# Optimization experiments

Measured on AMD Instinct MI355X. Metric: run time of the kernel, lower is better.

The kernel has to match this reference:

```python
import jax, jax.numpy as jnp
import numpy as np

B, T, N, D, H, S, L, O = 32, 12, 2048, 2, 64, 2, 2, 1


def setup_inputs() -> dict:
    key = jax.random.key(0)
    ks = jax.random.split(key, 32)
    inp = {}
    inp["x"] = jax.random.normal(ks[0], (B, T, N, D), dtype=jnp.float32)
    sup = jax.random.uniform(ks[1], (S, N, N), dtype=jnp.float32)
    # row-normalized, like random-walk diffusion transition matrices
    inp["supports"] = sup / jnp.sum(sup, axis=-1, keepdims=True)
    i = 2
    for l in range(L):
        din = (D if l == 0 else H) + H  # concat([x, h]) width
        for g in ("r", "u", "c"):
            inp[f"W{g}{l}"] = jax.random.normal(ks[i], (din, H), dtype=jnp.float32) * 0.02; i += 1
            inp[f"b{g}{l}"] = jnp.zeros((H,), jnp.float32)
        inp[f"Wd{l}"] = jax.random.normal(ks[i], (S, H, H), dtype=jnp.float32) * 0.02; i += 1
        inp[f"bd{l}"] = jnp.zeros((S, H), jnp.float32)
    inp["Wo"] = jax.random.normal(ks[i], (H, O), dtype=jnp.float32) * 0.02
    inp["bo"] = jnp.zeros((O,), jnp.float32)
    return inp


def _cell(x_t, h, supports, Wr, br, Wu, bu, Wc, bc, Wd, bd):
    # x_t: [B,N,din-H], h: [B,N,H]
    xh = jnp.concatenate([x_t, h], axis=-1)
    r = jax.nn.sigmoid(xh @ Wr + br)  # computed but unused, as in the source module
    u = jax.nn.sigmoid(xh @ Wu + bu)
    c = jnp.tanh(xh @ Wc + bc)
    # Diffusion conv is DEAD CODE in the source (h_diff never used); kept for fidelity,
    # DCE'd under jit. snm,bmh,shk -> per-support graph matmul + linear, summed.
    h_diff = h + jnp.einsum('snm,bmh,shk->bnk', supports, h, Wd) + jnp.sum(bd, axis=0)
    del r, h_diff
    return u * h + (1.0 - u) * c


def reference(x, supports,
              Wr0, br0, Wu0, bu0, Wc0, bc0, Wd0, bd0,
              Wr1, br1, Wu1, bu1, Wc1, bc1, Wd1, bd1,
              Wo, bo):
    p0 = (Wr0, br0, Wu0, bu0, Wc0, bc0, Wd0, bd0)
    p1 = (Wr1, br1, Wu1, bu1, Wc1, bc1, Wd1, bd1)

    def step(carry, x_t):
        h0, h1 = carry
        h0 = _cell(x_t, h0, supports, *p0)
        h1 = _cell(h0, h1, supports, *p1)  # dropout p=0.0 -> identity
        return (h0, h1), None

    h_init = (jnp.zeros((B, N, H), x.dtype), jnp.zeros((B, N, H), x.dtype))
    (h0, h1), _ = jax.lax.scan(step, h_init, jnp.swapaxes(x, 0, 1))  # scan over T
    return h1 @ Wo + bo  # [B, N, O]
```

## Files before the change

kernel.cpp:

```cpp
#include <hip/hip_runtime.h>


#define TSTEPS 12

__device__ __forceinline__ float fsig(float z) {
    z = fminf(fmaxf(z, -30.f), 30.f);
    return 1.f / (1.f + __expf(-z));
}
__device__ __forceinline__ float ftanh(float z) {
    z = fminf(fmaxf(z, -15.f), 15.f);
    float e = __expf(2.f * z);
    return 1.f - 2.f / (e + 1.f);
}


__global__ void pack_weights(const float* __restrict__ Wu0, const float* __restrict__ bu0,
                             const float* __restrict__ Wc0, const float* __restrict__ bc0,
                             const float* __restrict__ Wu1, const float* __restrict__ bu1,
                             const float* __restrict__ Wc1, const float* __restrict__ bc1,
                             const float* __restrict__ Wo, const float* __restrict__ bo,
                             float* __restrict__ Wp) {
    const int tid = blockIdx.x * blockDim.x + threadIdx.x;
    const int nthr = gridDim.x * blockDim.x;
    for (int i = tid; i < 256; i += nthr) {
        const int k = i >> 7, r = i & 127, wv = r >> 5, j = r & 31;
        const int col = wv * 16 + (j & 15);
        Wp[i] = (j < 16) ? Wu0[k * 64 + col] : Wc0[k * 64 + col];
    }
    for (int i = tid; i < 8192; i += nthr) {
        const int k = i >> 7, r = i & 127, wv = r >> 5, j = r & 31;
        const int col = wv * 16 + (j & 15);
        Wp[256 + i] = (j < 16) ? Wu0[(2 + k) * 64 + col] : Wc0[(2 + k) * 64 + col];
    }
    for (int i = tid; i < 16384; i += nthr) {
        const int k = i >> 7, r = i & 127, wv = r >> 5, j = r & 31;
        const int col = wv * 16 + (j & 15);
        Wp[8448 + i] = (j < 16) ? Wu1[k * 64 + col] : Wc1[k * 64 + col];
    }
    for (int i = tid; i < 128; i += nthr) {
        const int wv = i >> 5, j = i & 31;
        const int col = wv * 16 + (j & 15);
        Wp[24832 + i] = (j < 16) ? bu0[col] : bc0[col];
        Wp[24960 + i] = (j < 16) ? bu1[col] : bc1[col];
    }
    for (int i = tid; i < 64; i += nthr) Wp[25088 + i] = Wo[i];
    if (tid == 0) Wp[25152] = bo[0];
}

#define REP16(X) X(0) X(1) X(2) X(3) X(4) X(5) X(6) X(7) \
                 X(8) X(9) X(10) X(11) X(12) X(13) X(14) X(15)

#define INITJ(J) zu##J = bp_[J]; zc##J = bp_[16 + J];
#define FMAJ(J)  zu##J = __builtin_fmaf(hk_, wk_[J], zu##J); \
                 zc##J = __builtin_fmaf(hk_, wk_[16 + J], zc##J);
#define XPJ(J)   zu##J = __builtin_fmaf(xv.x, wx_[J], zu##J); \
                 zu##J = __builtin_fmaf(xv.y, wx_[128 + J], zu##J); \
                 zc##J = __builtin_fmaf(xv.x, wx_[16 + J], zc##J); \
                 zc##J = __builtin_fmaf(xv.y, wx_[128 + 16 + J], zc##J);
#define ACTJ(J)  { const float u_ = fsig(zu##J); const float c_ = ftanh(zc##J); \
                   zu##J = __builtin_fmaf(u_, hb_[(J) * 64], (1.f - u_) * c_); }
#define STJ(J)   hb_[(J) * 64] = zu##J;
#define KSTEP(AR, WB, KK) { const float hk_ = (AR)[(KK) * 64]; \
                            const float* wk_ = (WB) + (size_t)(KK) * 128; REP16(FMAJ) }
#define POJ(J)   part = __builtin_fmaf(zu##J, wo_[J], part);

__global__ __launch_bounds__(256, 4) void dcrnn_main(const float* __restrict__ x,
                                                     const float* __restrict__ Wp,
                                                     float* __restrict__ out) {
    __shared__ float A[128 * 64];
    __shared__ float P[4 * 64];

    const int tid = threadIdx.x;
    const int lane = tid & 63;
    const int w = __builtin_amdgcn_readfirstlane(tid >> 6);

    const int s0 = blockIdx.x * 64;
    const int b = s0 >> 11;
    const int n0 = s0 & 2047;

    const float* Wxw = Wp + w * 32;
    const float* W0w = Wp + 256 + w * 32;
    const float* W1w = Wp + 8448 + w * 32;
    const float* B0w = Wp + 24832 + w * 32;
    const float* B1w = Wp + 24960 + w * 32;

    for (int i = tid; i < 128 * 64; i += 256) A[i] = 0.f;
    __syncthreads();

    const float* Arow = A + lane;
    const float* xlane = x + (size_t)(b * TSTEPS) * 4096 + (size_t)(n0 + lane) * 2;
    float* hb0 = &A[(w * 16) * 64 + lane];
    float* hb1 = &A[(64 + w * 16) * 64 + lane];

    float zu0, zu1, zu2, zu3, zu4, zu5, zu6, zu7;
    float zu8, zu9, zu10, zu11, zu12, zu13, zu14, zu15;
    float zc0, zc1, zc2, zc3, zc4, zc5, zc6, zc7;
    float zc8, zc9, zc10, zc11, zc12, zc13, zc14, zc15;

#pragma unroll 1
    for (int t = 0; t < TSTEPS; ++t) {
        const float2 xv = *(const float2*)(xlane + t * 4096);

        { const float* bp_ = B0w; REP16(INITJ) }
#pragma unroll 1
        for (int k = 0; k < 64; k += 4) {
            KSTEP(Arow, W0w, k + 0)
            KSTEP(Arow, W0w, k + 1)
            KSTEP(Arow, W0w, k + 2)
            KSTEP(Arow, W0w, k + 3)
        }
        { const float* wx_ = Wxw; REP16(XPJ) }
        { const float* hb_ = hb0; REP16(ACTJ) }
        __syncthreads();
        { float* hb_ = hb0; REP16(STJ) }
        __syncthreads();

        { const float* bp_ = B1w; REP16(INITJ) }
#pragma unroll 1
        for (int k = 0; k < 128; k += 4) {
            KSTEP(Arow, W1w, k + 0)
            KSTEP(Arow, W1w, k + 1)
            KSTEP(Arow, W1w, k + 2)
            KSTEP(Arow, W1w, k + 3)
        }
        { const float* hb_ = hb1; REP16(ACTJ) }
        __syncthreads();
        { float* hb_ = hb1; REP16(STJ) }
    }

    float part = 0.f;
    { const float* wo_ = Wp + 25088 + w * 16; REP16(POJ) }
    P[w * 64 + lane] = part;
    __syncthreads();
    if (tid < 64) {
        out[s0 + tid] = Wp[25152] + P[tid] + P[64 + tid] + P[128 + tid] + P[192 + tid];
    }
}

extern "C" void kernel_launch(void* const* d_in, const int* in_sizes, int n_in,
                              void* d_out, int out_size, void* d_ws, size_t ws_size,
                              hipStream_t stream) {
    const float* x   = (const float*)d_in[0];
    const float* Wu0 = (const float*)d_in[4];
    const float* bu0 = (const float*)d_in[5];
    const float* Wc0 = (const float*)d_in[6];
    const float* bc0 = (const float*)d_in[7];
    const float* Wu1 = (const float*)d_in[12];
    const float* bu1 = (const float*)d_in[13];
    const float* Wc1 = (const float*)d_in[14];
    const float* bc1 = (const float*)d_in[15];
    const float* Wo  = (const float*)d_in[18];
    const float* bo  = (const float*)d_in[19];

    float* Wp = (float*)d_ws;

    hipLaunchKernelGGL(pack_weights, dim3(64), dim3(256), 0, stream,
                       Wu0, bu0, Wc0, bc0, Wu1, bu1, Wc1, bc1, Wo, bo, Wp);
    hipLaunchKernelGGL(dcrnn_main, dim3(65536 / 64), dim3(256), 0, stream,
                       x, Wp, (float*)d_out);
}
```

Measured before the change: 635.1 us.

## Retile GRU kernel to two nodes per lane and eight output columns per wave

Each block now handles 128 nodes with 512 threads. Each lane owns two adjacent nodes and each wave owns 8 of the 64 hidden columns, where before it was one node and 16 columns. Every weight scalar loaded from global/constant memory is now reused across two nodes, and shared-memory hidden-state reads become float2. This halves per-node weight-load traffic, at the cost of doubling shared memory per block (64KB), which may reduce how many blocks fit on each CU.

```diff
diff --git a/kernel.cpp b/kernel.cpp
--- a/kernel.cpp
+++ b/kernel.cpp
@@ -22,118 +22,146 @@
                              float* __restrict__ Wp) {
     const int tid = blockIdx.x * blockDim.x + threadIdx.x;
     const int nthr = gridDim.x * blockDim.x;
+    for (int i = tid; i < 8192; i += nthr) {
+        const int k = i >> 7, r = i & 127, wv = r >> 4, j = r & 15;
+        const int col = wv * 8 + (j & 7);
+        Wp[i] = (j < 8) ? Wu0[(2 + k) * 64 + col] : Wc0[(2 + k) * 64 + col];
+    }
     for (int i = tid; i < 256; i += nthr) {
-        const int k = i >> 7, r = i & 127, wv = r >> 5, j = r & 31;
-        const int col = wv * 16 + (j & 15);
-        Wp[i] = (j < 16) ? Wu0[k * 64 + col] : Wc0[k * 64 + col];
-    }
-    for (int i = tid; i < 8192; i += nthr) {
-        const int k = i >> 7, r = i & 127, wv = r >> 5, j = r & 31;
-        const int col = wv * 16 + (j & 15);
-        Wp[256 + i] = (j < 16) ? Wu0[(2 + k) * 64 + col] : Wc0[(2 + k) * 64 + col];
+        const int k = i >> 7, r = i & 127, wv = r >> 4, j = r & 15;
+        const int col = wv * 8 + (j & 7);
+        Wp[8192 + i] = (j < 8) ? Wu0[k * 64 + col] : Wc0[k * 64 + col];
     }
     for (int i = tid; i < 16384; i += nthr) {
-        const int k = i >> 7, r = i & 127, wv = r >> 5, j = r & 31;
-        const int col = wv * 16 + (j & 15);
-        Wp[8448 + i] = (j < 16) ? Wu1[k * 64 + col] : Wc1[k * 64 + col];
+        const int k = i >> 7, r = i & 127, wv = r >> 4, j = r & 15;
+        const int col = wv * 8 + (j & 7);
+        Wp[8448 + i] = (j < 8) ? Wu1[k * 64 + col] : Wc1[k * 64 + col];
     }
     for (int i = tid; i < 128; i += nthr) {
-        const int wv = i >> 5, j = i & 31;
-        const int col = wv * 16 + (j & 15);
-        Wp[24832 + i] = (j < 16) ? bu0[col] : bc0[col];
-        Wp[24960 + i] = (j < 16) ? bu1[col] : bc1[col];
+        const int wv = i >> 4, j = i & 15;
+        const int col = wv * 8 + (j & 7);
+        Wp[24832 + i] = (j < 8) ? bu0[col] : bc0[col];
+        Wp[24960 + i] = (j < 8) ? bu1[col] : bc1[col];
     }
     for (int i = tid; i < 64; i += nthr) Wp[25088 + i] = Wo[i];
     if (tid == 0) Wp[25152] = bo[0];
 }
 
-#define REP16(X) X(0) X(1) X(2) X(3) X(4) X(5) X(6) X(7) \
-                 X(8) X(9) X(10) X(11) X(12) X(13) X(14) X(15)
+#define REP8(X) X(0) X(1) X(2) X(3) X(4) X(5) X(6) X(7)
 
-#define INITJ(J) zu##J = bp_[J]; zc##J = bp_[16 + J];
-#define FMAJ(J)  zu##J = __builtin_fmaf(hk_, wk_[J], zu##J); \
-                 zc##J = __builtin_fmaf(hk_, wk_[16 + J], zc##J);
-#define XPJ(J)   zu##J = __builtin_fmaf(xv.x, wx_[J], zu##J); \
-                 zu##J = __builtin_fmaf(xv.y, wx_[128 + J], zu##J); \
-                 zc##J = __builtin_fmaf(xv.x, wx_[16 + J], zc##J); \
-                 zc##J = __builtin_fmaf(xv.y, wx_[128 + 16 + J], zc##J);
-#define ACTJ(J)  { const float u_ = fsig(zu##J); const float c_ = ftanh(zc##J); \
-                   zu##J = __builtin_fmaf(u_, hb_[(J) * 64], (1.f - u_) * c_); }
-#define STJ(J)   hb_[(J) * 64] = zu##J;
-#define KSTEP(AR, WB, KK) { const float hk_ = (AR)[(KK) * 64]; \
-                            const float* wk_ = (WB) + (size_t)(KK) * 128; REP16(FMAJ) }
-#define POJ(J)   part = __builtin_fmaf(zu##J, wo_[J], part);
+#define INITJ(J) zu##J##0 = bp_[J]; zu##J##1 = bp_[J]; \
+                 zc##J##0 = bp_[8 + J]; zc##J##1 = bp_[8 + J];
 
-__global__ __launch_bounds__(256, 4) void dcrnn_main(const float* __restrict__ x,
+#define FMAJ(J) \
+    zu##J##0 = __builtin_fmaf(hv.x, wk_[J], zu##J##0); \
+    zu##J##1 = __builtin_fmaf(hv.y, wk_[J], zu##J##1); \
+    zc##J##0 = __builtin_fmaf(hv.x, wk_[8 + J], zc##J##0); \
+    zc##J##1 = __builtin_fmaf(hv.y, wk_[8 + J], zc##J##1);
+
+#define KSTEP(WB, KK) { \
+    const float2 hv = *(const float2*)(Aptr + (size_t)(KK) * 128); \
+    const float* wk_ = (WB) + (size_t)(KK) * 128; \
+    REP8(FMAJ) }
+
+#define XPJ(J) \
+    zu##J##0 = __builtin_fmaf(xv.x, wx_[J], __builtin_fmaf(xv.y, wx_[128 + J], zu##J##0)); \
+    zu##J##1 = __builtin_fmaf(xv.z, wx_[J], __builtin_fmaf(xv.w, wx_[128 + J], zu##J##1)); \
+    zc##J##0 = __builtin_fmaf(xv.x, wx_[8 + J], __builtin_fmaf(xv.y, wx_[136 + J], zc##J##0)); \
+    zc##J##1 = __builtin_fmaf(xv.z, wx_[8 + J], __builtin_fmaf(xv.w, wx_[136 + J], zc##J##1));
+
+#define ACTJ(J) { \
+    const float2 ho = *(const float2*)(hb_ + (J) * 128); \
+    float u_, c_; \
+    u_ = fsig(zu##J##0); c_ = ftanh(zc##J##0); \
+    zu##J##0 = __builtin_fmaf(u_, ho.x, (1.f - u_) * c_); \
+    u_ = fsig(zu##J##1); c_ = ftanh(zc##J##1); \
+    zu##J##1 = __builtin_fmaf(u_, ho.y, (1.f - u_) * c_); }
+
+#define STJ(J) *(float2*)(hb_ + (J) * 128) = make_float2(zu##J##0, zu##J##1);
+
+#define POJ(J) part0 = __builtin_fmaf(zu##J##0, wo_[J], part0); \
+               part1 = __builtin_fmaf(zu##J##1, wo_[J], part1);
+
+__global__ __launch_bounds__(512, 4) void dcrnn_main(const float* __restrict__ x,
                                                      const float* __restrict__ Wp,
                                                      float* __restrict__ out) {
-    __shared__ float A[128 * 64];
-    __shared__ float P[4 * 64];
+    __shared__ float A[128 * 128];
+    __shared__ float P[8 * 128];
 
     const int tid = threadIdx.x;
     const int lane = tid & 63;
     const int w = __builtin_amdgcn_readfirstlane(tid >> 6);
 
-    const int s0 = blockIdx.x * 64;
+    const int s0 = blockIdx.x * 128;
     const int b = s0 >> 11;
     const int n0 = s0 & 2047;
 
-    const float* Wxw = Wp + w * 32;
-    const float* W0w = Wp + 256 + w * 32;
-    const float* W1w = Wp + 8448 + w * 32;
-    const float* B0w = Wp + 24832 + w * 32;
-    const float* B1w = Wp + 24960 + w * 32;
+    const float* W0w = Wp + w * 16;
+    const float* Wxw = Wp + 8192 + w * 16;
+    const float* W1w = Wp + 8448 + w * 16;
+    const float* B0w = Wp + 24832 + w * 16;
+    const float* B1w = Wp + 24960 + w * 16;
 
-    for (int i = tid; i < 128 * 64; i += 256) A[i] = 0.f;
+    for (int i = tid; i < 128 * 128; i += 512) A[i] = 0.f;
     __syncthreads();
 
-    const float* Arow = A + lane;
-    const float* xlane = x + (size_t)(b * TSTEPS) * 4096 + (size_t)(n0 + lane) * 2;
-    float* hb0 = &A[(w * 16) * 64 + lane];
-    float* hb1 = &A[(64 + w * 16) * 64 + lane];
+    const float* Aptr0 = A + 2 * lane;
+    float* hb0 = A + (size_t)(w * 8) * 128 + 2 * lane;
+    float* hb1 = A + (size_t)(64 + w * 8) * 128 + 2 * lane;
 
-    float zu0, zu1, zu2, zu3, zu4, zu5, zu6, zu7;
-    float zu8, zu9, zu10, zu11, zu12, zu13, zu14, zu15;
-    float zc0, zc1, zc2, zc3, zc4, zc5, zc6, zc7;
-    float zc8, zc9, zc10, zc11, zc12, zc13, zc14, zc15;
+    const float* xlane = x + (size_t)(b * TSTEPS) * 4096 + (size_t)(n0 + 2 * lane) * 2;
+
+    float zu00, zu01, zu10, zu11, zu20, zu21, zu30, zu31;
+    float zu40, zu41, zu50, zu51, zu60, zu61, zu70, zu71;
+    float zc00, zc01, zc10, zc11, zc20, zc21, zc30, zc31;
+    float zc40, zc41, zc50, zc51, zc60, zc61, zc70, zc71;
 
 #pragma unroll 1
     for (int t = 0; t < TSTEPS; ++t) {
-        const float2 xv = *(const float2*)(xlane + t * 4096);
+        const float4 xv = *(const float4*)(xlane + (size_t)t * 4096);
 
-        { const float* bp_ = B0w; REP16(INITJ) }
+        { const float* bp_ = B0w; REP8(INITJ) }
+        {
+            const float* Aptr = Aptr0;
 #pragma unroll 1
-        for (int k = 0; k < 64; k += 4) {
-            KSTEP(Arow, W0w, k + 0)
-            KSTEP(Arow, W0w, k + 1)
-            KSTEP(Arow, W0w, k + 2)
-            KSTEP(Arow, W0w, k + 3)
+            for (int k = 0; k < 64; k += 4) {
+                KSTEP(W0w, k + 0)
+                KSTEP(W0w, k + 1)
+                KSTEP(W0w, k + 2)
+                KSTEP(W0w, k + 3)
+            }
         }
-        { const float* wx_ = Wxw; REP16(XPJ) }
-        { const float* hb_ = hb0; REP16(ACTJ) }
+        { const float* wx_ = Wxw; REP8(XPJ) }
+        { const float* hb_ = hb0; REP8(ACTJ) }
         __syncthreads();
-        { float* hb_ = hb0; REP16(STJ) }
+        { float* hb_ = hb0; REP8(STJ) }
         __syncthreads();
 
-        { const float* bp_ = B1w; REP16(INITJ) }
+        { const float* bp_ = B1w; REP8(INITJ) }
+        {
+            const float* Aptr = Aptr0;
 #pragma unroll 1
-        for (int k = 0; k < 128; k += 4) {
-            KSTEP(Arow, W1w, k + 0)
-            KSTEP(Arow, W1w, k + 1)
-            KSTEP(Arow, W1w, k + 2)
-            KSTEP(Arow, W1w, k + 3)
+            for (int k = 0; k < 128; k += 4) {
+                KSTEP(W1w, k + 0)
+                KSTEP(W1w, k + 1)
+                KSTEP(W1w, k + 2)
+                KSTEP(W1w, k + 3)
+            }
         }
-        { const float* hb_ = hb1; REP16(ACTJ) }
+        { const float* hb_ = hb1; REP8(ACTJ) }
         __syncthreads();
-        { float* hb_ = hb1; REP16(STJ) }
+        { float* hb_ = hb1; REP8(STJ) }
     }
 
-    float part = 0.f;
-    { const float* wo_ = Wp + 25088 + w * 16; REP16(POJ) }
-    P[w * 64 + lane] = part;
+    float part0 = 0.f, part1 = 0.f;
+    { const float* wo_ = Wp + 25088 + w * 8; REP8(POJ) }
+    *(float2*)&P[w * 128 + 2 * lane] = make_float2(part0, part1);
     __syncthreads();
-    if (tid < 64) {
-        out[s0 + tid] = Wp[25152] + P[tid] + P[64 + tid] + P[128 + tid] + P[192 + tid];
+    if (tid < 128) {
+        float acc = Wp[25152];
+#pragma unroll
+        for (int wv = 0; wv < 8; ++wv) acc += P[wv * 128 + tid];
+        out[s0 + tid] = acc;
     }
 }
 
@@ -156,6 +184,6 @@
 
     hipLaunchKernelGGL(pack_weights, dim3(64), dim3(256), 0, stream,
                        Wu0, bu0, Wc0, bc0, Wu1, bu1, Wc1, bc1, Wo, bo, Wp);
-    hipLaunchKernelGGL(dcrnn_main, dim3(65536 / 64), dim3(256), 0, stream,
+    hipLaunchKernelGGL(dcrnn_main, dim3(65536 / 128), dim3(512), 0, stream,
                        x, Wp, (float*)d_out);
 }
```

New measurement: 589.1 us. 7.2% less time.

## Skew the two GRU layers into one pass per step with 2-node register tiles

Applied to the files above, without the earlier changes.

Layer 1 at step t-1 now runs in the same pass as layer 0 at step t. Both read the hidden state in shared memory from the previous pass, which cuts the barriers per step from three to two and lets one shared-memory read feed both layers. Each block now covers 128 nodes with 1024 threads, and each thread computes 2 nodes by 4 columns with float2 and float4 loads, so each weight load is reused across two nodes. The cost is one extra pass at the end, more registers per thread, and a reworked weight packing.

```diff
diff --git a/kernel.cpp b/kernel.cpp
--- a/kernel.cpp
+++ b/kernel.cpp
@@ -18,122 +18,165 @@
                              const float* __restrict__ Wc0, const float* __restrict__ bc0,
                              const float* __restrict__ Wu1, const float* __restrict__ bu1,
                              const float* __restrict__ Wc1, const float* __restrict__ bc1,
-                             const float* __restrict__ Wo, const float* __restrict__ bo,
                              float* __restrict__ Wp) {
     const int tid = blockIdx.x * blockDim.x + threadIdx.x;
     const int nthr = gridDim.x * blockDim.x;
+    for (int i = tid; i < 16384; i += nthr) {
+        const int k = i >> 8, r = i & 255, wv = r >> 4, j = r & 15;
+        const int col = wv * 4 + (j & 3);
+        float v;
+        if (j < 4)       v = Wu0[(2 + k) * 64 + col];
+        else if (j < 8)  v = Wc0[(2 + k) * 64 + col];
+        else if (j < 12) v = Wu1[k * 64 + col];
+        else             v = Wc1[k * 64 + col];
+        Wp[i] = v;
+    }
+    for (int i = tid; i < 8192; i += nthr) {
+        const int k = i >> 7, r = i & 127, wv = r >> 3, j = r & 7;
+        const int col = wv * 4 + (j & 3);
+        Wp[16384 + i] = (j < 4) ? Wu1[(64 + k) * 64 + col] : Wc1[(64 + k) * 64 + col];
+    }
     for (int i = tid; i < 256; i += nthr) {
-        const int k = i >> 7, r = i & 127, wv = r >> 5, j = r & 31;
-        const int col = wv * 16 + (j & 15);
-        Wp[i] = (j < 16) ? Wu0[k * 64 + col] : Wc0[k * 64 + col];
-    }
-    for (int i = tid; i < 8192; i += nthr) {
-        const int k = i >> 7, r = i & 127, wv = r >> 5, j = r & 31;
-        const int col = wv * 16 + (j & 15);
-        Wp[256 + i] = (j < 16) ? Wu0[(2 + k) * 64 + col] : Wc0[(2 + k) * 64 + col];
-    }
-    for (int i = tid; i < 16384; i += nthr) {
-        const int k = i >> 7, r = i & 127, wv = r >> 5, j = r & 31;
-        const int col = wv * 16 + (j & 15);
-        Wp[8448 + i] = (j < 16) ? Wu1[k * 64 + col] : Wc1[k * 64 + col];
+        const int k = i >> 7, r = i & 127, wv = r >> 3, j = r & 7;
+        const int col = wv * 4 + (j & 3);
+        Wp[24576 + i] = (j < 4) ? Wu0[k * 64 + col] : Wc0[k * 64 + col];
     }
     for (int i = tid; i < 128; i += nthr) {
-        const int wv = i >> 5, j = i & 31;
-        const int col = wv * 16 + (j & 15);
-        Wp[24832 + i] = (j < 16) ? bu0[col] : bc0[col];
-        Wp[24960 + i] = (j < 16) ? bu1[col] : bc1[col];
-    }
-    for (int i = tid; i < 64; i += nthr) Wp[25088 + i] = Wo[i];
-    if (tid == 0) Wp[25152] = bo[0];
-}
-
-#define REP16(X) X(0) X(1) X(2) X(3) X(4) X(5) X(6) X(7) \
-                 X(8) X(9) X(10) X(11) X(12) X(13) X(14) X(15)
-
-#define INITJ(J) zu##J = bp_[J]; zc##J = bp_[16 + J];
-#define FMAJ(J)  zu##J = __builtin_fmaf(hk_, wk_[J], zu##J); \
-                 zc##J = __builtin_fmaf(hk_, wk_[16 + J], zc##J);
-#define XPJ(J)   zu##J = __builtin_fmaf(xv.x, wx_[J], zu##J); \
-                 zu##J = __builtin_fmaf(xv.y, wx_[128 + J], zu##J); \
-                 zc##J = __builtin_fmaf(xv.x, wx_[16 + J], zc##J); \
-                 zc##J = __builtin_fmaf(xv.y, wx_[128 + 16 + J], zc##J);
-#define ACTJ(J)  { const float u_ = fsig(zu##J); const float c_ = ftanh(zc##J); \
-                   zu##J = __builtin_fmaf(u_, hb_[(J) * 64], (1.f - u_) * c_); }
-#define STJ(J)   hb_[(J) * 64] = zu##J;
-#define KSTEP(AR, WB, KK) { const float hk_ = (AR)[(KK) * 64]; \
-                            const float* wk_ = (WB) + (size_t)(KK) * 128; REP16(FMAJ) }
-#define POJ(J)   part = __builtin_fmaf(zu##J, wo_[J], part);
-
-__global__ __launch_bounds__(256, 4) void dcrnn_main(const float* __restrict__ x,
-                                                     const float* __restrict__ Wp,
-                                                     float* __restrict__ out) {
-    __shared__ float A[128 * 64];
-    __shared__ float P[4 * 64];
+        const int wv = i >> 3, j = i & 7;
+        const int col = wv * 4 + (j & 3);
+        Wp[24832 + i] = (j < 4) ? bu0[col] : bc0[col];
+        Wp[24960 + i] = (j < 4) ? bu1[col] : bc1[col];
+    }
+}
+
+#define F(a, b, c) __builtin_fmaf((a), (b), (c))
+
+#define FMA8(U0, U1, U2, U3, HV, W) \
+    U0##0 = F(HV.x, W.x, U0##0); U0##1 = F(HV.y, W.x, U0##1); \
+    U1##0 = F(HV.x, W.y, U1##0); U1##1 = F(HV.y, W.y, U1##1); \
+    U2##0 = F(HV.x, W.z, U2##0); U2##1 = F(HV.y, W.z, U2##1); \
+    U3##0 = F(HV.x, W.w, U3##0); U3##1 = F(HV.y, W.w, U3##1);
+
+#define KLO(KK) { \
+    const float2 hv = *(const float2*)(Ab + (KK) * 128); \
+    const float4 q0 = WLo[(KK) * 64 + 0], q1 = WLo[(KK) * 64 + 1]; \
+    FMA8(aU0, aU1, aU2, aU3, hv, q0) \
+    FMA8(aC0, aC1, aC2, aC3, hv, q1) \
+    const float4 q2 = WLo[(KK) * 64 + 2], q3 = WLo[(KK) * 64 + 3]; \
+    FMA8(bU0, bU1, bU2, bU3, hv, q2) \
+    FMA8(bC0, bC1, bC2, bC3, hv, q3) }
+
+#define KHI(KK) { \
+    const float2 hv = *(const float2*)(Ab + (64 + (KK)) * 128); \
+    const float4 q2 = WHi[(KK) * 32 + 0], q3 = WHi[(KK) * 32 + 1]; \
+    FMA8(bU0, bU1, bU2, bU3, hv, q2) \
+    FMA8(bC0, bC1, bC2, bC3, hv, q3) }
+
+#define ZSET(A0, A1, A2, A3, V) A0##0 = V.x; A0##1 = V.x; A1##0 = V.y; A1##1 = V.y; \
+                                A2##0 = V.z; A2##1 = V.z; A3##0 = V.w; A3##1 = V.w;
+
+#define ACT0(J) { \
+    const float2 ho = *(const float2*)(A + (w4 + (J)) * 128 + 2 * lane); \
+    float u_, c_; \
+    u_ = fsig(aU##J##0); c_ = ftanh(aC##J##0); hn0_##J.x = F(u_, ho.x, (1.f - u_) * c_); \
+    u_ = fsig(aU##J##1); c_ = ftanh(aC##J##1); hn0_##J.y = F(u_, ho.y, (1.f - u_) * c_); }
+
+#define ACT1(J) { \
+    const float2 ho = *(const float2*)(A + (64 + w4 + (J)) * 128 + 2 * lane); \
+    float u_, c_; \
+    u_ = fsig(bU##J##0); c_ = ftanh(bC##J##0); hn1_##J.x = F(u_, ho.x, (1.f - u_) * c_); \
+    u_ = fsig(bU##J##1); c_ = ftanh(bC##J##1); hn1_##J.y = F(u_, ho.y, (1.f - u_) * c_); }
+
+__global__ __launch_bounds__(1024, 8) void dcrnn_main(const float* __restrict__ x,
+                                                      const float* __restrict__ Wp,
+                                                      const float* __restrict__ Wo,
+                                                      const float* __restrict__ bo,
+                                                      float* __restrict__ out) {
+    __shared__ float A[128 * 128];
 
     const int tid = threadIdx.x;
     const int lane = tid & 63;
-    const int w = __builtin_amdgcn_readfirstlane(tid >> 6);
-
-    const int s0 = blockIdx.x * 64;
+    const int w = tid >> 6;
+    const int w4 = w * 4;
+
+    const int s0 = blockIdx.x * 128;
     const int b = s0 >> 11;
     const int n0 = s0 & 2047;
 
-    const float* Wxw = Wp + w * 32;
-    const float* W0w = Wp + 256 + w * 32;
-    const float* W1w = Wp + 8448 + w * 32;
-    const float* B0w = Wp + 24832 + w * 32;
-    const float* B1w = Wp + 24960 + w * 32;
-
-    for (int i = tid; i < 128 * 64; i += 256) A[i] = 0.f;
+    const float4* WLo = (const float4*)Wp + w * 4;
+    const float4* WHi = (const float4*)(Wp + 16384) + w * 2;
+    const float4* WX  = (const float4*)(Wp + 24576) + w * 2;
+    const float4* B0p = (const float4*)(Wp + 24832) + w * 2;
+    const float4* B1p = (const float4*)(Wp + 24960) + w * 2;
+
+    for (int i = tid; i < 128 * 128; i += 1024) A[i] = 0.f;
     __syncthreads();
 
-    const float* Arow = A + lane;
-    const float* xlane = x + (size_t)(b * TSTEPS) * 4096 + (size_t)(n0 + lane) * 2;
-    float* hb0 = &A[(w * 16) * 64 + lane];
-    float* hb1 = &A[(64 + w * 16) * 64 + lane];
-
-    float zu0, zu1, zu2, zu3, zu4, zu5, zu6, zu7;
-    float zu8, zu9, zu10, zu11, zu12, zu13, zu14, zu15;
-    float zc0, zc1, zc2, zc3, zc4, zc5, zc6, zc7;
-    float zc8, zc9, zc10, zc11, zc12, zc13, zc14, zc15;
+    const float* Ab = A + 2 * lane;
+    const float* xlane = x + (size_t)b * (TSTEPS * 4096) + (size_t)(n0 + 2 * lane) * 2;
+
+    float aU00, aU01, aU10, aU11, aU20, aU21, aU30, aU31;
+    float aC00, aC01, aC10, aC11, aC20, aC21, aC30, aC31;
+    float bU00, bU01, bU10, bU11, bU20, bU21, bU30, bU31;
+    float bC00, bC01, bC10, bC11, bC20, bC21, bC30, bC31;
+    float2 hn0_0, hn0_1, hn0_2, hn0_3;
+    float2 hn1_0, hn1_1, hn1_2, hn1_3;
 
 #pragma unroll 1
-    for (int t = 0; t < TSTEPS; ++t) {
-        const float2 xv = *(const float2*)(xlane + t * 4096);
-
-        { const float* bp_ = B0w; REP16(INITJ) }
-#pragma unroll 1
-        for (int k = 0; k < 64; k += 4) {
-            KSTEP(Arow, W0w, k + 0)
-            KSTEP(Arow, W0w, k + 1)
-            KSTEP(Arow, W0w, k + 2)
-            KSTEP(Arow, W0w, k + 3)
-        }
-        { const float* wx_ = Wxw; REP16(XPJ) }
-        { const float* hb_ = hb0; REP16(ACTJ) }
+    for (int p = 0; p < TSTEPS + 1; ++p) {
+        const int xt = (p < TSTEPS) ? p : (TSTEPS - 1);
+
+        {
+            const float4 v0 = B0p[0], v1 = B0p[1];
+            ZSET(aU0, aU1, aU2, aU3, v0)
+            ZSET(aC0, aC1, aC2, aC3, v1)
+            const float4 v2 = B1p[0], v3 = B1p[1];
+            ZSET(bU0, bU1, bU2, bU3, v2)
+            ZSET(bC0, bC1, bC2, bC3, v3)
+        }
+
+#pragma unroll 4
+        for (int k = 0; k < 64; ++k) { KLO(k) }
+
+        {
+            const float4 xv = *(const float4*)(xlane + (size_t)xt * 4096);
+            const float4 q0 = WX[0], q1 = WX[1];
+            const float4 q2 = WX[32], q3 = WX[33];
+            const float2 x0 = make_float2(xv.x, xv.z);
+            const float2 x1 = make_float2(xv.y, xv.w);
+            FMA8(aU0, aU1, aU2, aU3, x0, q0)
+            FMA8(aC0, aC1, aC2, aC3, x0, q1)
+            FMA8(aU0, aU1, aU2, aU3, x1, q2)
+            FMA8(aC0, aC1, aC2, aC3, x1, q3)
+        }
+        ACT0(0) ACT0(1) ACT0(2) ACT0(3)
+
+#pragma unroll 4
+        for (int k = 0; k < 64; ++k) { KHI(k) }
+        ACT1(0) ACT1(1) ACT1(2) ACT1(3)
+
         __syncthreads();
-        { float* hb_ = hb0; REP16(STJ) }
+        if (p < TSTEPS) {
+            *(float2*)(A + (w4 + 0) * 128 + 2 * lane) = hn0_0;
+            *(float2*)(A + (w4 + 1) * 128 + 2 * lane) = hn0_1;
+            *(float2*)(A + (w4 + 2) * 128 + 2 * lane) = hn0_2;
+            *(float2*)(A + (w4 + 3) * 128 + 2 * lane) = hn0_3;
+        }
+        if (p >= 1) {
+            *(float2*)(A + (64 + w4 + 0) * 128 + 2 * lane) = hn1_0;
+            *(float2*)(A + (64 + w4 + 1) * 128 + 2 * lane) = hn1_1;
+            *(float2*)(A + (64 + w4 + 2) * 128 + 2 * lane) = hn1_2;
+            *(float2*)(A + (64 + w4 + 3) * 128 + 2 * lane) = hn1_3;
+        }
         __syncthreads();
-
-        { const float* bp_ = B1w; REP16(INITJ) }
-#pragma unroll 1
-        for (int k = 0; k < 128; k += 4) {
-            KSTEP(Arow, W1w, k + 0)
-            KSTEP(Arow, W1w, k + 1)
-            KSTEP(Arow, W1w, k + 2)
-            KSTEP(Arow, W1w, k + 3)
-        }
-        { const float* hb_ = hb1; REP16(ACTJ) }
-        __syncthreads();
-        { float* hb_ = hb1; REP16(STJ) }
-    }
-
-    float part = 0.f;
-    { const float* wo_ = Wp + 25088 + w * 16; REP16(POJ) }
-    P[w * 64 + lane] = part;
-    __syncthreads();
-    if (tid < 64) {
-        out[s0 + tid] = Wp[25152] + P[tid] + P[64 + tid] + P[128 + tid] + P[192 + tid];
+    }
+
+    if (tid < 128) {
+        float acc = bo[0];
+#pragma unroll 8
+        for (int k = 0; k < 64; ++k)
+            acc = F(A[(64 + k) * 128 + tid], Wo[k], acc);
+        out[s0 + tid] = acc;
     }
 }
 
@@ -155,7 +198,7 @@
     float* Wp = (float*)d_ws;
 
     hipLaunchKernelGGL(pack_weights, dim3(64), dim3(256), 0, stream,
-                       Wu0, bu0, Wc0, bc0, Wu1, bu1, Wc1, bc1, Wo, bo, Wp);
-    hipLaunchKernelGGL(dcrnn_main, dim3(65536 / 64), dim3(256), 0, stream,
-                       x, Wp, (float*)d_out);
-}
+                       Wu0, bu0, Wc0, bc0, Wu1, bu1, Wc1, bc1, Wp);
+    hipLaunchKernelGGL(dcrnn_main, dim3(65536 / 128), dim3(1024), 0, stream,
+                       x, Wp, Wo, bo, (float*)d_out);
+}
```

Result: slower. 1.964 ms (+209.2%).
